# Kernel tuning notes

Measured on AMD Instinct MI355X. Metric: run time of the kernel, lower is better.

The kernel has to match this reference:

```python
import jax, jax.numpy as jnp
import numpy as np

N_NODES = 50000
N_EDGES = 1600000
NUM_GRAPHS = 512
HID = 128
EDGE_DIM = 64
N_CONV = 4
BN_EPS = 1e-5


def setup_inputs() -> dict:
    key = jax.random.key(0)
    ks = jax.random.split(key, 16)
    x = jax.random.normal(ks[0], (N_NODES, 9), dtype=jnp.float32)
    edge_index = jax.random.randint(ks[1], (2, N_EDGES), 0, N_NODES, dtype=jnp.int64)
    edge_attr = jax.random.normal(ks[2], (N_EDGES, EDGE_DIM), dtype=jnp.float32)
    batch = jnp.sort(jax.random.randint(ks[3], (N_NODES,), 0, NUM_GRAPHS, dtype=jnp.int64))
    s = 0.05
    W_emb = jax.random.normal(ks[4], (9, HID), dtype=jnp.float32) * s
    b_emb = jnp.zeros((HID,), jnp.float32)
    zin = 2 * HID + EDGE_DIM  # 320: cat([x_i, x_j, edge_attr])
    Wf = jax.random.normal(ks[5], (N_CONV, zin, HID), dtype=jnp.float32) * s
    bf = jnp.zeros((N_CONV, HID), jnp.float32)
    Ws = jax.random.normal(ks[6], (N_CONV, zin, HID), dtype=jnp.float32) * s
    bs = jnp.zeros((N_CONV, HID), jnp.float32)
    gamma = jnp.ones((N_CONV, HID), jnp.float32)
    beta = jnp.zeros((N_CONV, HID), jnp.float32)
    W1 = jax.random.normal(ks[7], (HID, HID // 2), dtype=jnp.float32) * s
    b1 = jnp.zeros((HID // 2,), jnp.float32)
    W2 = jax.random.normal(ks[8], (HID // 2, 1), dtype=jnp.float32) * s
    b2 = jnp.zeros((1,), jnp.float32)
    return dict(x=x, edge_index=edge_index, edge_attr=edge_attr, batch=batch,
                W_emb=W_emb, b_emb=b_emb, Wf=Wf, bf=bf, Ws=Ws, bs=bs,
                gamma=gamma, beta=beta, W1=W1, b1=b1, W2=W2, b2=b2)


def _segment_mean(vals, idx, num_segments):
    s = jax.ops.segment_sum(vals, idx, num_segments=num_segments)
    cnt = jax.ops.segment_sum(jnp.ones((vals.shape[0], 1), vals.dtype), idx,
                              num_segments=num_segments)
    return s / jnp.maximum(cnt, 1.0)


def _forward(x, edge_index, edge_attr, batch, W_emb, b_emb, Wf, bf, Ws, bs,
             gamma, beta, W1, b1, W2, b2):
    src, dst = edge_index[0], edge_index[1]  # x_j = x[src], x_i = x[dst]
    h = x @ W_emb + b_emb  # [N, HID]
    for l in range(N_CONV):
        residual = h
        # lin(cat([x_i, x_j, e])) == x_i@W[:H] + x_j@W[H:2H] + e@W[2H:] + b,
        # with node projections done at N granularity before the edge gather.
        f = (h @ Wf[l, :HID])[dst] + (h @ Wf[l, HID:2 * HID])[src] \
            + edge_attr @ Wf[l, 2 * HID:] + bf[l]
        g = (h @ Ws[l, :HID])[dst] + (h @ Ws[l, HID:2 * HID])[src] \
            + edge_attr @ Ws[l, 2 * HID:] + bs[l]
        msg = jax.nn.sigmoid(f) * jax.nn.softplus(g)  # [E, HID]
        aggr = _segment_mean(msg, dst, N_NODES)
        h_conv = aggr + h  # CGConv internal residual
        # BatchNorm1d (training-mode batch stats, biased variance)
        mu = jnp.mean(h_conv, axis=0)
        var = jnp.mean(jnp.square(h_conv - mu), axis=0)
        h_bn = gamma[l] * (h_conv - mu) * jax.lax.rsqrt(var + BN_EPS) + beta[l]
        h = jax.nn.relu(h_bn) + residual  # dropout = identity (eval)
    pooled = _segment_mean(h, batch, NUM_GRAPHS)  # [G, HID]
    out = jax.nn.softplus(pooled @ W1 + b1) @ W2 + b2
    return out.squeeze(-1)  # [G]


def reference(x, edge_index, edge_attr, batch, W_emb, b_emb, Wf, bf, Ws, bs,
              gamma, beta, W1, b1, W2, b2):
    return _forward(x, edge_index, edge_attr, batch, W_emb, b_emb, Wf, bf,
                    Ws, bs, gamma, beta, W1, b1, W2, b2)
```

## Files before the change

kernel.cpp:

```cpp
#include <hip/hip_runtime.h>
#include <math.h>

#define N_NODES 50000
#define N_EDGES 1600000
#define NGRAPH  512
#define HID     128
#define EDIM    64
#define NCONV   4

typedef __attribute__((ext_vector_type(8))) short short8;
typedef __attribute__((ext_vector_type(4))) float f32x4;
typedef unsigned int  u32;
typedef unsigned short u16;

#define MFMA16(a, b, c) __builtin_amdgcn_mfma_f32_16x16x32_bf16(a, b, c, 0, 0, 0)

__device__ __forceinline__ float fsig(float x) {
  return __builtin_amdgcn_rcpf(1.f + __expf(-x));
}
__device__ __forceinline__ float fsp(float x) {
  return fmaxf(x, 0.f) + __logf(1.f + __expf(-fabsf(x)));
}
__device__ __forceinline__ u16 f2bf(float x) {
  u32 u = __float_as_uint(x);
  return (u16)((u + 0x7fff + ((u >> 16) & 1)) >> 16);
}
__device__ __forceinline__ u32 f2bf_pack(float lo, float hi) {
  u32 a = __float_as_uint(lo), b = __float_as_uint(hi);
  u32 ra = (a + 0x7fff + ((a >> 16) & 1)) >> 16;
  u32 rb = (b + 0x7fff + ((b >> 16) & 1)) & 0xffff0000u;
  return ra | rb;
}
__device__ __forceinline__ short8 cvt8(float4 a, float4 b) {
  union { short8 s; u32 u[4]; } r;
  r.u[0] = f2bf_pack(a.x, a.y);
  r.u[1] = f2bf_pack(a.z, a.w);
  r.u[2] = f2bf_pack(b.x, b.y);
  r.u[3] = f2bf_pack(b.z, b.w);
  return r.s;
}

__global__ __launch_bounds__(256) void k_embed(const float* __restrict__ x,
                                               const float* __restrict__ Wemb,
                                               const float* __restrict__ bemb,
                                               float* __restrict__ h,
                                               u16* __restrict__ hb, u16* __restrict__ hlo) {
  int i = blockIdx.x * blockDim.x + threadIdx.x;
  if (i >= N_NODES * HID) return;
  int n = i >> 7, c = i & 127;
  const float* xr = x + (size_t)n * 9;
  float acc = bemb[c];
#pragma unroll
  for (int k = 0; k < 9; k++) acc = fmaf(xr[k], Wemb[k * HID + c], acc);
  h[i] = acc;
  u16 hi16 = f2bf(acc);
  hb[i] = hi16;
  hlo[i] = f2bf(acc - __uint_as_float((u32)hi16 << 16));
}

__global__ __launch_bounds__(256) void k_count(const int* __restrict__ ei, int* __restrict__ cnt) {
  int e = blockIdx.x * blockDim.x + threadIdx.x;
  if (e >= N_EDGES) return;
  atomicAdd(&cnt[ei[N_EDGES + e]], 1);
}

__global__ __launch_bounds__(256) void k_scan1(const int* __restrict__ cnt, int* __restrict__ bsum) {
  __shared__ int s[256];
  int i = blockIdx.x * 256 + threadIdx.x;
  s[threadIdx.x] = (i < N_NODES) ? cnt[i] : 0;
  __syncthreads();
  for (int o = 128; o > 0; o >>= 1) {
    if (threadIdx.x < o) s[threadIdx.x] += s[threadIdx.x + o];
    __syncthreads();
  }
  if (threadIdx.x == 0) bsum[blockIdx.x] = s[0];
}

__global__ __launch_bounds__(256) void k_scan2(int* __restrict__ bsum, int nb) {
  __shared__ int s[256];
  int tid = threadIdx.x;
  s[tid] = (tid < nb) ? bsum[tid] : 0;
  __syncthreads();
  for (int o = 1; o < 256; o <<= 1) {
    int t = (tid >= o) ? s[tid - o] : 0;
    __syncthreads();
    s[tid] += t;
    __syncthreads();
  }
  if (tid < nb) bsum[tid] = (tid == 0) ? 0 : s[tid - 1];
}

__global__ __launch_bounds__(256) void k_scan3(const int* __restrict__ cnt, const int* __restrict__ bsum,
                                               int* __restrict__ row_start, float* __restrict__ inv) {
  __shared__ int s[256];
  int i = blockIdx.x * 256 + threadIdx.x;
  int v = (i < N_NODES) ? cnt[i] : 0;
  s[threadIdx.x] = v;
  __syncthreads();
  for (int o = 1; o < 256; o <<= 1) {
    int t = (threadIdx.x >= o) ? s[threadIdx.x - o] : 0;
    __syncthreads();
    s[threadIdx.x] += t;
    __syncthreads();
  }
  if (i < N_NODES) {
    row_start[i + 1] = s[threadIdx.x] + bsum[blockIdx.x];
    inv[i] = 1.0f / (float)max(v, 1);
    if (i == 0) row_start[0] = 0;
  }
}

__global__ __launch_bounds__(256) void k_fill(const int* __restrict__ ei, const int* __restrict__ row_start,
                                              int* __restrict__ cur, int* __restrict__ eids,
                                              int* __restrict__ esrc) {
  int e = blockIdx.x * blockDim.x + threadIdx.x;
  if (e < 64) {
    eids[N_EDGES + e] = 0;
    esrc[N_EDGES + e] = 0;
  }
  if (e >= N_EDGES) return;
  int s = ei[e], d = ei[N_EDGES + e];
  int pos = row_start[d] + atomicAdd(&cur[d], 1);
  eids[pos] = e;
  esrc[pos] = s;
}

__global__ __launch_bounds__(256) void k_gatherA(const float* __restrict__ eattr,
                                                 const int* __restrict__ eids,
                                                 u16* __restrict__ Ae) {
  int t = blockIdx.x * 256 + threadIdx.x;
  if (t >= (N_EDGES + 64) * 8) return;
  int pos = t >> 3, chunk = t & 7;
  short8* dst = (short8*)((char*)Ae + ((size_t)pos << 7) + (chunk << 4));
  if (pos >= N_EDGES) {
    union { short8 s; u32 u[4]; } z; z.u[0] = z.u[1] = z.u[2] = z.u[3] = 0;
    *dst = z.s;
    return;
  }
  int eid = eids[pos];
  const float* src = eattr + ((size_t)eid << 6) + (chunk << 3);
  float4 a = *(const float4*)src;
  float4 b = *(const float4*)(src + 4);
  *dst = cvt8(a, b);
}

__global__ __launch_bounds__(256) void k_prepW(const float* __restrict__ Wf,
                                               const float* __restrict__ Ws,
                                               u16* __restrict__ Whi, u16* __restrict__ Wlo) {
  int t = blockIdx.x * 256 + threadIdx.x;
  if (t >= 65536 * NCONV) return;
  int l = t >> 16, t16 = t & 65535;
  int c = t16 >> 7, k = t16 & 127;
  int q = c >> 7, col = c & 127;
  const float* W = ((q < 2) ? Wf : Ws) + (size_t)l * 320 * HID;
  int row = (q & 1) ? (128 + k) : k;
  float wv = W[row * HID + col];
  u16 hb16 = f2bf(wv);
  float lo = wv - __uint_as_float((u32)hb16 << 16);
  int nt = (c >> 4) & 7, l15 = c & 15;
  int s = k >> 5, lg = (k >> 3) & 3, i = k & 7;
  int idx = l * 65536 + (((q * 8 + nt) * 4 + s) * 64 + (lg * 16 + l15)) * 8 + i;
  Whi[idx] = hb16;
  Wlo[idx] = f2bf(lo);
}

__global__ __launch_bounds__(256) void k_prepB(const float* __restrict__ Wf,
                                               const float* __restrict__ Ws,
                                               u16* __restrict__ Bhi) {
  int t = blockIdx.x * 256 + threadIdx.x;
  if (t >= 16384 * NCONV) return;
  int l = t >> 14, tid = t & 16383;
  int i = tid & 7, lane = (tid >> 3) & 63, s = (tid >> 9) & 1, nt = tid >> 10;
  int k = s * 32 + ((lane >> 4) << 3) + i;
  int col = ((nt & 7) << 4) + (lane & 15);
  const float* W = ((nt < 8) ? Wf : Ws) + (size_t)l * 320 * HID + 256 * HID;
  Bhi[t] = f2bf(W[k * HID + col]);
}

__global__ __launch_bounds__(256) void k_nodeproj_mfma(
    const u16* __restrict__ hb, const u16* __restrict__ hlo,
    const u16* __restrict__ Whi, const u16* __restrict__ Wlo,
    const float* __restrict__ bf_l, const float* __restrict__ bs_l,
    float* __restrict__ Pd, u32* __restrict__ Ppk) {
  const int lane = threadIdx.x & 63, w = threadIdx.x >> 6;
  const int l15 = lane & 15, lg = lane >> 4;
  const int nb = blockIdx.x * 16;
  const short8* WH = (const short8*)Whi;
  const short8* WL = (const short8*)Wlo;
  f32x4 acc[8];
#pragma unroll
  for (int nt = 0; nt < 8; nt++) acc[nt] = (f32x4){0.f, 0.f, 0.f, 0.f};
  const u32 arow = ((u32)(nb + l15)) << 8;
#pragma unroll
  for (int s = 0; s < 4; s++) {
    u32 ao = arow + (s << 6) + (lg << 4);
    short8 ah = *(const short8*)((const char*)hb + ao);
    short8 al = *(const short8*)((const char*)hlo + ao);
#pragma unroll
    for (int nt = 0; nt < 8; nt++) {
      int bi = ((w * 8 + nt) * 4 + s) * 64 + lane;
      short8 bhv = WH[bi];
      short8 blv = WL[bi];
      acc[nt] = MFMA16(ah, bhv, acc[nt]);
      acc[nt] = MFMA16(ah, blv, acc[nt]);
      acc[nt] = MFMA16(al, bhv, acc[nt]);
    }
  }
  if ((w & 1) == 0) {
    const float* bias = (w == 0) ? bf_l : bs_l;
    int pdoff = (w == 0) ? 0 : 128;
#pragma unroll
    for (int nt = 0; nt < 8; nt++) {
      int col = nt * 16 + l15;
      float b = bias[col];
#pragma unroll
      for (int r = 0; r < 4; r++) {
        int node = nb + lg * 4 + r;
        Pd[(size_t)node * 256 + pdoff + col] = acc[nt][r] + b;
      }
    }
  } else {
    int off = (w == 1) ? 0 : 1;
#pragma unroll
    for (int g = 0; g < 4; g++) {
#pragma unroll
      for (int r = 0; r < 4; r++) {
        int node = nb + lg * 4 + r;
        Ppk[(size_t)node * 128 + 2 * (g * 16 + l15) + off] =
            f2bf_pack(acc[2 * g][r], acc[2 * g + 1][r]);
      }
    }
  }
}

__global__ __launch_bounds__(256, 5) void k_edge_mfma(
    const float* __restrict__ Pd, const u32* __restrict__ Ppk,
    const float* __restrict__ h, const u16* __restrict__ Ae,
    const int* __restrict__ row_start, const float* __restrict__ inv,
    const int* __restrict__ esrc, const u16* __restrict__ Bhi,
    float* __restrict__ hconv, float* __restrict__ stats) {
  const int tid = threadIdx.x;
  const int lane = tid & 63;
  const int w = tid >> 6;
  const int l15 = lane & 15, lg = lane >> 4;
  const int cb = w * 32;

  const short8* BH = (const short8*)Bhi;
  short8 bh[4][2];
  const int nts[4] = {2 * w, 2 * w + 1, 8 + 2 * w, 9 + 2 * w};
#pragma unroll
  for (int t = 0; t < 4; t++) {
#pragma unroll
    for (int s = 0; s < 2; s++) bh[t][s] = BH[(nts[t] * 2 + s) * 64 + lane];
  }

  const u32 poff = ((u32)(w * 16 + l15)) << 3;
  const int eoff = lg << 2;
  const char* aeb = (const char*)Ae;
  const char* ppb = (const char*)Ppk;

  float st0s = 0.f, st0q = 0.f, st1s = 0.f, st1q = 0.f;

  for (int node = blockIdx.x; node < N_NODES; node += gridDim.x) {
    int rs = row_start[node], re = row_start[node + 1];
    int deg = re - rs;
    if (deg == 0) {
      if (lane < 32) {
        size_t idx = (size_t)node * HID + cb + lane;
        float v = h[idx];
        hconv[idx] = v;
        if (lane < 16) { st0s += v; st0q += v * v; }
        else           { st1s += v; st1q += v * v; }
      }
      continue;
    }
    const float* Pn = Pd + (size_t)node * 256;
    float fd0 = Pn[cb + l15];
    float fd1 = Pn[cb + 16 + l15];
    float gd0 = Pn[128 + cb + l15];
    float gd1 = Pn[128 + cb + 16 + l15];
    float acc0 = 0.f, acc1 = 0.f;
    int ntile = (deg + 15) >> 4;

    const int* ep = esrc + rs + eoff;
    int sn0 = ep[0], sn1 = ep[1], sn2 = ep[2], sn3 = ep[3];
    uint2 gc0 = *(const uint2*)(ppb + (((u32)sn0) << 9) + poff);
    uint2 gc1 = *(const uint2*)(ppb + (((u32)sn1) << 9) + poff);
    uint2 gc2 = *(const uint2*)(ppb + (((u32)sn2) << 9) + poff);
    uint2 gc3 = *(const uint2*)(ppb + (((u32)sn3) << 9) + poff);
    sn0 = ep[16]; sn1 = ep[17]; sn2 = ep[18]; sn3 = ep[19];
    u32 ab = ((u32)(rs + l15) << 7) + ((u32)lg << 4);
    short8 ac0 = *(const short8*)(aeb + ab);
    short8 ac1 = *(const short8*)(aeb + ab + 64);

    for (int mt = 0; mt < ntile; mt++) {
      uint2 gn0 = *(const uint2*)(ppb + (((u32)sn0) << 9) + poff);
      uint2 gn1 = *(const uint2*)(ppb + (((u32)sn1) << 9) + poff);
      uint2 gn2 = *(const uint2*)(ppb + (((u32)sn2) << 9) + poff);
      uint2 gn3 = *(const uint2*)(ppb + (((u32)sn3) << 9) + poff);
      int t2 = (mt + 2) * 16;
      sn0 = ep[t2 + 0]; sn1 = ep[t2 + 1]; sn2 = ep[t2 + 2]; sn3 = ep[t2 + 3];

      f32x4 d0 = {fd0, fd0, fd0, fd0};
      f32x4 d1 = {fd1, fd1, fd1, fd1};
      f32x4 d2 = {gd0, gd0, gd0, gd0};
      f32x4 d3 = {gd1, gd1, gd1, gd1};
      d0 = MFMA16(ac0, bh[0][0], d0); d0 = MFMA16(ac1, bh[0][1], d0);
      d1 = MFMA16(ac0, bh[1][0], d1); d1 = MFMA16(ac1, bh[1][1], d1);
      d2 = MFMA16(ac0, bh[2][0], d2); d2 = MFMA16(ac1, bh[2][1], d2);
      d3 = MFMA16(ac0, bh[3][0], d3); d3 = MFMA16(ac1, bh[3][1], d3);

      u32 ab1 = ab + (u32)(mt + 1) * 2048;
      ac0 = *(const short8*)(aeb + ab1);
      ac1 = *(const short8*)(aeb + ab1 + 64);

      const uint2 pgr[4] = {gc0, gc1, gc2, gc3};
      bool fullt = ((mt + 1) * 16 <= deg);
#pragma unroll
      for (int r = 0; r < 4; r++) {
        uint2 pg = pgr[r];
        float f0 = d0[r] + __uint_as_float(pg.x << 16);
        float f1 = d1[r] + __uint_as_float(pg.x & 0xffff0000u);
        float g0 = d2[r] + __uint_as_float(pg.y << 16);
        float g1 = d3[r] + __uint_as_float(pg.y & 0xffff0000u);
        float m0 = fsig(f0) * fsp(g0);
        float m1 = fsig(f1) * fsp(g1);
        if (!fullt) {
          int row = mt * 16 + (lg << 2) + r;
          if (row >= deg) { m0 = 0.f; m1 = 0.f; }
        }
        acc0 += m0;
        acc1 += m1;
      }
      gc0 = gn0; gc1 = gn1; gc2 = gn2; gc3 = gn3;
    }
    acc0 += __shfl_xor(acc0, 16); acc0 += __shfl_xor(acc0, 32);
    acc1 += __shfl_xor(acc1, 16); acc1 += __shfl_xor(acc1, 32);
    float iv = inv[node];
    if (lane < 16) {
      size_t idx = (size_t)node * HID + cb + lane;
      float v = acc0 * iv + h[idx];
      hconv[idx] = v;
      st0s += v; st0q += v * v;
    } else if (lane < 32) {
      size_t idx = (size_t)node * HID + cb + 16 + l15;
      float v = acc1 * iv + h[idx];
      hconv[idx] = v;
      st1s += v; st1q += v * v;
    }
  }
  if (lane < 16) {
    atomicAdd(&stats[cb + lane], st0s);
    atomicAdd(&stats[128 + cb + lane], st0q);
  } else if (lane < 32) {
    atomicAdd(&stats[cb + 16 + l15], st1s);
    atomicAdd(&stats[128 + cb + 16 + l15], st1q);
  }
}

__global__ __launch_bounds__(256) void k_bn3(const float* __restrict__ hconv, float* __restrict__ h,
                                             const float* __restrict__ stats,
                                             const float* __restrict__ gamma,
                                             const float* __restrict__ beta,
                                             u16* __restrict__ hb, u16* __restrict__ hlo) {
  __shared__ float ssl[256];
  int t = threadIdx.x;
  if (t < 128) {
    float mu = stats[t] * (1.f / N_NODES);
    float var = stats[128 + t] * (1.f / N_NODES) - mu * mu;
    float sc = gamma[t] * rsqrtf(var + 1e-5f);
    ssl[t] = sc;
    ssl[128 + t] = beta[t] - mu * sc;
  }
  __syncthreads();
  int i = blockIdx.x * 256 + t;
  if (i >= N_NODES * HID) return;
  int c = i & 127;
  float v = hconv[i] * ssl[c] + ssl[128 + c];
  float hn = fmaxf(v, 0.f) + h[i];
  h[i] = hn;
  u16 hi16 = f2bf(hn);
  hb[i] = hi16;
  hlo[i] = f2bf(hn - __uint_as_float((u32)hi16 << 16));
}

__global__ __launch_bounds__(128) void k_pool(const float* __restrict__ h, const int* __restrict__ batch,
                                              float* __restrict__ pooled) {
  int g = blockIdx.x;
  int c = threadIdx.x;
  int lo = 0, hi = N_NODES;
  while (lo < hi) { int m = (lo + hi) >> 1; if (batch[m] < g) lo = m + 1; else hi = m; }
  int s = lo;
  lo = 0; hi = N_NODES;
  while (lo < hi) { int m = (lo + hi) >> 1; if (batch[m] < g + 1) lo = m + 1; else hi = m; }
  int e = lo;
  float acc = 0.f;
  for (int n = s; n < e; n++) acc += h[(size_t)n * HID + c];
  pooled[(size_t)g * HID + c] = acc / (float)max(e - s, 1);
}

__global__ __launch_bounds__(64) void k_head(const float* __restrict__ pooled, const float* __restrict__ W1,
                                             const float* __restrict__ b1, const float* __restrict__ W2,
                                             const float* __restrict__ b2, float* __restrict__ out) {
  int g = blockIdx.x;
  int j = threadIdx.x;
  float acc = b1[j];
#pragma unroll 16
  for (int k = 0; k < 128; k++) acc = fmaf(pooled[(size_t)g * HID + k], W1[k * 64 + j], acc);
  float z = fmaxf(acc, 0.f) + __logf(1.f + __expf(-fabsf(acc)));
  float v = z * W2[j];
  for (int o = 32; o > 0; o >>= 1) v += __shfl_down(v, o);
  if (j == 0) out[g] = v + b2[0];
}

extern "C" void kernel_launch(void* const* d_in, const int* in_sizes, int n_in,
                              void* d_out, int out_size, void* d_ws, size_t ws_size,
                              hipStream_t stream) {
  const float* x     = (const float*)d_in[0];
  const int*   ei    = (const int*)d_in[1];
  const float* eattr = (const float*)d_in[2];
  const int*   batch = (const int*)d_in[3];
  const float* Wemb  = (const float*)d_in[4];
  const float* bemb  = (const float*)d_in[5];
  const float* Wf    = (const float*)d_in[6];
  const float* bf    = (const float*)d_in[7];
  const float* Ws    = (const float*)d_in[8];
  const float* bs    = (const float*)d_in[9];
  const float* gamma = (const float*)d_in[10];
  const float* beta  = (const float*)d_in[11];
  const float* W1    = (const float*)d_in[12];
  const float* b1    = (const float*)d_in[13];
  const float* W2    = (const float*)d_in[14];
  const float* b2    = (const float*)d_in[15];
  float* out = (float*)d_out;

  char* ws = (char*)d_ws;
  size_t off = 0;
  auto alloc = [&](size_t bytes) -> char* {
    char* p = ws + off;
    off += (bytes + 255) & ~(size_t)255;
    return p;
  };
  float* h         = (float*)alloc((size_t)N_NODES * HID * 4);
  u16*   hb        = (u16*)alloc((size_t)N_NODES * HID * 2);
  u16*   hlo       = (u16*)alloc((size_t)N_NODES * HID * 2);
  float* Pd        = (float*)alloc((size_t)N_NODES * 256 * 4);
  u32*   Ppk       = (u32*)alloc((size_t)N_NODES * 128 * 4);
  float* hconv     = (float*)alloc((size_t)N_NODES * HID * 4);
  int*   row_start = (int*)alloc((size_t)(N_NODES + 1) * 4);
  float* inv       = (float*)alloc((size_t)N_NODES * 4);
  int*   eids      = (int*)alloc((size_t)(N_EDGES + 64) * 4);
  int*   esrc      = (int*)alloc((size_t)(N_EDGES + 64) * 4);
  u16*   Ae        = (u16*)alloc((size_t)(N_EDGES + 64) * EDIM * 2);
  u16*   Bhi       = (u16*)alloc((size_t)16384 * NCONV * 2);
  u16*   Whi       = (u16*)alloc((size_t)65536 * NCONV * 2);
  u16*   Wlo       = (u16*)alloc((size_t)65536 * NCONV * 2);
  char*  zbase     = ws + off;
  int*   cnt       = (int*)alloc((size_t)N_NODES * 4);
  int*   cur       = (int*)alloc((size_t)N_NODES * 4);
  float* stats     = (float*)alloc((size_t)NCONV * 256 * 4);
  size_t zbytes    = (size_t)((ws + off) - zbase);
  int*   bsum      = (int*)alloc(256 * 4);
  float* pooled    = (float*)alloc((size_t)NGRAPH * HID * 4);
  (void)ws_size; (void)in_sizes; (void)n_in; (void)out_size;

  hipMemsetAsync(zbase, 0, zbytes, stream);

  k_embed<<<(N_NODES * HID + 255) / 256, 256, 0, stream>>>(x, Wemb, bemb, h, hb, hlo);

  k_count<<<(N_EDGES + 255) / 256, 256, 0, stream>>>(ei, cnt);
  int nb = (N_NODES + 255) / 256;
  k_scan1<<<nb, 256, 0, stream>>>(cnt, bsum);
  k_scan2<<<1, 256, 0, stream>>>(bsum, nb);
  k_scan3<<<nb, 256, 0, stream>>>(cnt, bsum, row_start, inv);
  k_fill<<<(N_EDGES + 255) / 256, 256, 0, stream>>>(ei, row_start, cur, eids, esrc);
  k_gatherA<<<((N_EDGES + 64) * 8 + 255) / 256, 256, 0, stream>>>(eattr, eids, Ae);
  k_prepW<<<65536 * NCONV / 256, 256, 0, stream>>>(Wf, Ws, Whi, Wlo);
  k_prepB<<<16384 * NCONV / 256, 256, 0, stream>>>(Wf, Ws, Bhi);

  for (int l = 0; l < NCONV; l++) {
    k_nodeproj_mfma<<<N_NODES / 16, 256, 0, stream>>>(hb, hlo, Whi + l * 65536, Wlo + l * 65536,
                                                      bf + l * HID, bs + l * HID, Pd, Ppk);
    k_edge_mfma<<<2560, 256, 0, stream>>>(Pd, Ppk, h, Ae, row_start, inv, esrc,
                                          Bhi + l * 16384, hconv, stats + l * 256);
    k_bn3<<<(N_NODES * HID + 255) / 256, 256, 0, stream>>>(hconv, h, stats + l * 256,
                                                           gamma + l * HID, beta + l * HID,
                                                           hb, hlo);
  }

  k_pool<<<NGRAPH, HID, 0, stream>>>(h, batch, pooled);
  k_head<<<NGRAPH, 64, 0, stream>>>(pooled, W1, b1, W2, b2, out);
}
```

Before: 2.192 ms.

## Balance edge kernel with 16-edge tile worklist and atomic aggregation

Replaces the per-node grid-stride edge loop with a precomputed worklist of 16-edge tiles, built once per forward by scan kernels. Each block then gets a contiguous, equal-sized chunk of tiles, which removes load imbalance from varying node degree. Partial sums are flushed with atomics into a zeroed aggr buffer, and a separate k_stats kernel applies the mean, adds the residual and computes BN statistics. The cost is an extra memset and an extra pass over hconv per layer, atomic traffic at node boundaries, and a lower occupancy hint.

```diff
diff --git a/kernel.cpp b/kernel.cpp
--- a/kernel.cpp
+++ b/kernel.cpp
@@ -7,6 +7,7 @@
 #define HID     128
 #define EDIM    64
 #define NCONV   4
+#define MAXWI   150064
 
 typedef __attribute__((ext_vector_type(8))) short short8;
 typedef __attribute__((ext_vector_type(4))) float f32x4;
@@ -123,6 +124,55 @@
   int pos = row_start[d] + atomicAdd(&cur[d], 1);
   eids[pos] = e;
   esrc[pos] = s;
+}
+
+__global__ __launch_bounds__(256) void k_tilecnt(const int* __restrict__ row_start,
+                                                 int* __restrict__ tcnt) {
+  int i = blockIdx.x * 256 + threadIdx.x;
+  if (i >= N_NODES) return;
+  tcnt[i] = (row_start[i + 1] - row_start[i] + 15) >> 4;
+}
+
+__global__ __launch_bounds__(256) void k_scan3w(const int* __restrict__ tcnt,
+                                                const int* __restrict__ bsum,
+                                                int* __restrict__ tstart) {
+  __shared__ int s[256];
+  int i = blockIdx.x * 256 + threadIdx.x;
+  int v = (i < N_NODES) ? tcnt[i] : 0;
+  s[threadIdx.x] = v;
+  __syncthreads();
+  for (int o = 1; o < 256; o <<= 1) {
+    int t = (threadIdx.x >= o) ? s[threadIdx.x - o] : 0;
+    __syncthreads();
+    s[threadIdx.x] += t;
+    __syncthreads();
+  }
+  if (i < N_NODES) {
+    tstart[i] = s[threadIdx.x] - v + bsum[blockIdx.x];
+    if (i == N_NODES - 1) tstart[N_NODES] = s[threadIdx.x] + bsum[blockIdx.x];
+  }
+}
+
+__global__ __launch_bounds__(256) void k_wfill(const int* __restrict__ row_start,
+                                               const int* __restrict__ tstart,
+                                               int* __restrict__ wnode, int* __restrict__ wbase) {
+  int n = blockIdx.x * 256 + threadIdx.x;
+  if (n >= N_NODES) return;
+  int rs = row_start[n], re = row_start[n + 1];
+  int ts = tstart[n];
+  int nt = (re - rs + 15) >> 4;
+  for (int mt = 0; mt < nt; ++mt) {
+    wnode[ts + mt] = n;
+    wbase[ts + mt] = rs + mt * 16;
+  }
+}
+
+__global__ void k_wpad(const int* __restrict__ tstart,
+                       int* __restrict__ wnode, int* __restrict__ wbase) {
+  int t = threadIdx.x;
+  int nwi = tstart[N_NODES];
+  wnode[nwi + t] = 0;
+  wbase[nwi + t] = 0;
 }
 
 __global__ __launch_bounds__(256) void k_gatherA(const float* __restrict__ eattr,
@@ -233,18 +283,24 @@
   }
 }
 
-__global__ __launch_bounds__(256, 5) void k_edge_mfma(
+__global__ __launch_bounds__(256, 4) void k_edge_wl(
     const float* __restrict__ Pd, const u32* __restrict__ Ppk,
-    const float* __restrict__ h, const u16* __restrict__ Ae,
-    const int* __restrict__ row_start, const float* __restrict__ inv,
+    const u16* __restrict__ Ae, const int* __restrict__ row_start,
     const int* __restrict__ esrc, const u16* __restrict__ Bhi,
-    float* __restrict__ hconv, float* __restrict__ stats) {
+    const int* __restrict__ wnode, const int* __restrict__ wbase,
+    const int* __restrict__ tstart, float* __restrict__ aggr) {
   const int tid = threadIdx.x;
   const int lane = tid & 63;
   const int w = tid >> 6;
   const int l15 = lane & 15, lg = lane >> 4;
   const int cb = w * 32;
 
+  const int NWI = tstart[N_NODES];
+  int C = (NWI + (int)gridDim.x - 1) / (int)gridDim.x;
+  int k0 = (int)blockIdx.x * C;
+  int k1 = min(k0 + C, NWI);
+  if (k0 >= k1) return;
+
   const short8* BH = (const short8*)Bhi;
   short8 bh[4][2];
   const int nts[4] = {2 * w, 2 * w + 1, 8 + 2 * w, 9 + 2 * w};
@@ -259,102 +315,114 @@
   const char* aeb = (const char*)Ae;
   const char* ppb = (const char*)Ppk;
 
-  float st0s = 0.f, st0q = 0.f, st1s = 0.f, st1q = 0.f;
-
-  for (int node = blockIdx.x; node < N_NODES; node += gridDim.x) {
-    int rs = row_start[node], re = row_start[node + 1];
-    int deg = re - rs;
-    if (deg == 0) {
-      if (lane < 32) {
-        size_t idx = (size_t)node * HID + cb + lane;
-        float v = h[idx];
-        hconv[idx] = v;
-        if (lane < 16) { st0s += v; st0q += v * v; }
-        else           { st1s += v; st1q += v * v; }
+  int wn0 = wnode[k0],     wb0 = wbase[k0];
+  int wn1 = wnode[k0 + 1], wb1 = wbase[k0 + 1];
+  int wn2 = wnode[k0 + 2], wb2 = wbase[k0 + 2];
+  int re0 = row_start[wn0 + 1];
+  const float* Pn0 = Pd + (size_t)wn0 * 256;
+  float fd0 = Pn0[cb + l15], fd1 = Pn0[cb + 16 + l15];
+  float gd0 = Pn0[128 + cb + l15], gd1 = Pn0[128 + cb + 16 + l15];
+  uint2 gc0, gc1, gc2, gc3;
+  {
+    const int* ep0 = esrc + wb0 + eoff;
+    int a = ep0[0], b = ep0[1], c2 = ep0[2], d = ep0[3];
+    gc0 = *(const uint2*)(ppb + (((u32)a) << 9) + poff);
+    gc1 = *(const uint2*)(ppb + (((u32)b) << 9) + poff);
+    gc2 = *(const uint2*)(ppb + (((u32)c2) << 9) + poff);
+    gc3 = *(const uint2*)(ppb + (((u32)d) << 9) + poff);
+  }
+  const int* ep1 = esrc + wb1 + eoff;
+  int sA0 = ep1[0], sA1 = ep1[1], sA2 = ep1[2], sA3 = ep1[3];
+  u32 ab = ((u32)(wb0 + l15) << 7) + ((u32)lg << 4);
+  short8 ac0 = *(const short8*)(aeb + ab);
+  short8 ac1 = *(const short8*)(aeb + ab + 64);
+
+  float acc0 = 0.f, acc1 = 0.f;
+
+  for (int k = k0; k < k1; ++k) {
+    uint2 gn0 = *(const uint2*)(ppb + (((u32)sA0) << 9) + poff);
+    uint2 gn1 = *(const uint2*)(ppb + (((u32)sA1) << 9) + poff);
+    uint2 gn2 = *(const uint2*)(ppb + (((u32)sA2) << 9) + poff);
+    uint2 gn3 = *(const uint2*)(ppb + (((u32)sA3) << 9) + poff);
+    int wn3 = wnode[k + 3], wb3 = wbase[k + 3];
+    const int* ep2 = esrc + wb2 + eoff;
+    int t0 = ep2[0], t1 = ep2[1], t2 = ep2[2], t3 = ep2[3];
+    int re1 = row_start[wn1 + 1];
+    const float* Pn1 = Pd + (size_t)wn1 * 256;
+    float nfd0 = Pn1[cb + l15], nfd1 = Pn1[cb + 16 + l15];
+    float ngd0 = Pn1[128 + cb + l15], ngd1 = Pn1[128 + cb + 16 + l15];
+
+    f32x4 d0 = {fd0, fd0, fd0, fd0};
+    f32x4 d1 = {fd1, fd1, fd1, fd1};
+    f32x4 d2 = {gd0, gd0, gd0, gd0};
+    f32x4 d3 = {gd1, gd1, gd1, gd1};
+    d0 = MFMA16(ac0, bh[0][0], d0); d0 = MFMA16(ac1, bh[0][1], d0);
+    d1 = MFMA16(ac0, bh[1][0], d1); d1 = MFMA16(ac1, bh[1][1], d1);
+    d2 = MFMA16(ac0, bh[2][0], d2); d2 = MFMA16(ac1, bh[2][1], d2);
+    d3 = MFMA16(ac0, bh[3][0], d3); d3 = MFMA16(ac1, bh[3][1], d3);
+
+    u32 ab1 = ((u32)(wb1 + l15) << 7) + ((u32)lg << 4);
+    ac0 = *(const short8*)(aeb + ab1);
+    ac1 = *(const short8*)(aeb + ab1 + 64);
+
+    const uint2 pgr[4] = {gc0, gc1, gc2, gc3};
+    int rowlim = re0 - wb0;
+    bool fullt = (rowlim >= 16);
+#pragma unroll
+    for (int r = 0; r < 4; r++) {
+      uint2 pg = pgr[r];
+      float f0 = d0[r] + __uint_as_float(pg.x << 16);
+      float f1 = d1[r] + __uint_as_float(pg.x & 0xffff0000u);
+      float g0 = d2[r] + __uint_as_float(pg.y << 16);
+      float g1 = d3[r] + __uint_as_float(pg.y & 0xffff0000u);
+      float m0 = fsig(f0) * fsp(g0);
+      float m1 = fsig(f1) * fsp(g1);
+      if (!fullt) {
+        int row = (lg << 2) + r;
+        if (row >= rowlim) { m0 = 0.f; m1 = 0.f; }
       }
-      continue;
+      acc0 += m0;
+      acc1 += m1;
     }
-    const float* Pn = Pd + (size_t)node * 256;
-    float fd0 = Pn[cb + l15];
-    float fd1 = Pn[cb + 16 + l15];
-    float gd0 = Pn[128 + cb + l15];
-    float gd1 = Pn[128 + cb + 16 + l15];
-    float acc0 = 0.f, acc1 = 0.f;
-    int ntile = (deg + 15) >> 4;
-
-    const int* ep = esrc + rs + eoff;
-    int sn0 = ep[0], sn1 = ep[1], sn2 = ep[2], sn3 = ep[3];
-    uint2 gc0 = *(const uint2*)(ppb + (((u32)sn0) << 9) + poff);
-    uint2 gc1 = *(const uint2*)(ppb + (((u32)sn1) << 9) + poff);
-    uint2 gc2 = *(const uint2*)(ppb + (((u32)sn2) << 9) + poff);
-    uint2 gc3 = *(const uint2*)(ppb + (((u32)sn3) << 9) + poff);
-    sn0 = ep[16]; sn1 = ep[17]; sn2 = ep[18]; sn3 = ep[19];
-    u32 ab = ((u32)(rs + l15) << 7) + ((u32)lg << 4);
-    short8 ac0 = *(const short8*)(aeb + ab);
-    short8 ac1 = *(const short8*)(aeb + ab + 64);
-
-    for (int mt = 0; mt < ntile; mt++) {
-      uint2 gn0 = *(const uint2*)(ppb + (((u32)sn0) << 9) + poff);
-      uint2 gn1 = *(const uint2*)(ppb + (((u32)sn1) << 9) + poff);
-      uint2 gn2 = *(const uint2*)(ppb + (((u32)sn2) << 9) + poff);
-      uint2 gn3 = *(const uint2*)(ppb + (((u32)sn3) << 9) + poff);
-      int t2 = (mt + 2) * 16;
-      sn0 = ep[t2 + 0]; sn1 = ep[t2 + 1]; sn2 = ep[t2 + 2]; sn3 = ep[t2 + 3];
-
-      f32x4 d0 = {fd0, fd0, fd0, fd0};
-      f32x4 d1 = {fd1, fd1, fd1, fd1};
-      f32x4 d2 = {gd0, gd0, gd0, gd0};
-      f32x4 d3 = {gd1, gd1, gd1, gd1};
-      d0 = MFMA16(ac0, bh[0][0], d0); d0 = MFMA16(ac1, bh[0][1], d0);
-      d1 = MFMA16(ac0, bh[1][0], d1); d1 = MFMA16(ac1, bh[1][1], d1);
-      d2 = MFMA16(ac0, bh[2][0], d2); d2 = MFMA16(ac1, bh[2][1], d2);
-      d3 = MFMA16(ac0, bh[3][0], d3); d3 = MFMA16(ac1, bh[3][1], d3);
-
-      u32 ab1 = ab + (u32)(mt + 1) * 2048;
-      ac0 = *(const short8*)(aeb + ab1);
-      ac1 = *(const short8*)(aeb + ab1 + 64);
-
-      const uint2 pgr[4] = {gc0, gc1, gc2, gc3};
-      bool fullt = ((mt + 1) * 16 <= deg);
-#pragma unroll
-      for (int r = 0; r < 4; r++) {
-        uint2 pg = pgr[r];
-        float f0 = d0[r] + __uint_as_float(pg.x << 16);
-        float f1 = d1[r] + __uint_as_float(pg.x & 0xffff0000u);
-        float g0 = d2[r] + __uint_as_float(pg.y << 16);
-        float g1 = d3[r] + __uint_as_float(pg.y & 0xffff0000u);
-        float m0 = fsig(f0) * fsp(g0);
-        float m1 = fsig(f1) * fsp(g1);
-        if (!fullt) {
-          int row = mt * 16 + (lg << 2) + r;
-          if (row >= deg) { m0 = 0.f; m1 = 0.f; }
-        }
-        acc0 += m0;
-        acc1 += m1;
+
+    if (wn0 != wn1 || k == k1 - 1) {
+      acc0 += __shfl_xor(acc0, 16); acc0 += __shfl_xor(acc0, 32);
+      acc1 += __shfl_xor(acc1, 16); acc1 += __shfl_xor(acc1, 32);
+      if (lane < 16) {
+        atomicAdd(&aggr[(size_t)wn0 * HID + cb + lane], acc0);
+      } else if (lane < 32) {
+        atomicAdd(&aggr[(size_t)wn0 * HID + cb + 16 + l15], acc1);
       }
-      gc0 = gn0; gc1 = gn1; gc2 = gn2; gc3 = gn3;
+      acc0 = 0.f; acc1 = 0.f;
     }
-    acc0 += __shfl_xor(acc0, 16); acc0 += __shfl_xor(acc0, 32);
-    acc1 += __shfl_xor(acc1, 16); acc1 += __shfl_xor(acc1, 32);
-    float iv = inv[node];
-    if (lane < 16) {
-      size_t idx = (size_t)node * HID + cb + lane;
-      float v = acc0 * iv + h[idx];
-      hconv[idx] = v;
-      st0s += v; st0q += v * v;
-    } else if (lane < 32) {
-      size_t idx = (size_t)node * HID + cb + 16 + l15;
-      float v = acc1 * iv + h[idx];
-      hconv[idx] = v;
-      st1s += v; st1q += v * v;
-    }
-  }
-  if (lane < 16) {
-    atomicAdd(&stats[cb + lane], st0s);
-    atomicAdd(&stats[128 + cb + lane], st0q);
-  } else if (lane < 32) {
-    atomicAdd(&stats[cb + 16 + l15], st1s);
-    atomicAdd(&stats[128 + cb + 16 + l15], st1q);
+
+    wn0 = wn1; wb0 = wb1; wn1 = wn2; wb1 = wb2; wn2 = wn3; wb2 = wb3;
+    re0 = re1;
+    fd0 = nfd0; fd1 = nfd1; gd0 = ngd0; gd1 = ngd1;
+    gc0 = gn0; gc1 = gn1; gc2 = gn2; gc3 = gn3;
+    sA0 = t0; sA1 = t1; sA2 = t2; sA3 = t3;
+  }
+}
+
+__global__ __launch_bounds__(256) void k_stats(float* __restrict__ hconv,
+                                               const float* __restrict__ h,
+                                               const float* __restrict__ inv,
+                                               float* __restrict__ stats) {
+  __shared__ float sb[512];
+  int c = threadIdx.x & 127;
+  float s1 = 0.f, s2 = 0.f;
+  for (int i = blockIdx.x * 256 + threadIdx.x; i < N_NODES * HID; i += gridDim.x * 256) {
+    float v = hconv[i] * inv[i >> 7] + h[i];
+    hconv[i] = v;
+    s1 += v;
+    s2 += v * v;
+  }
+  sb[threadIdx.x] = s1;
+  sb[256 + threadIdx.x] = s2;
+  __syncthreads();
+  if (threadIdx.x < 128) {
+    atomicAdd(&stats[c], sb[threadIdx.x] + sb[threadIdx.x + 128]);
+    atomicAdd(&stats[128 + c], sb[256 + threadIdx.x] + sb[256 + threadIdx.x + 128]);
   }
 }
 
@@ -455,6 +523,11 @@
   u16*   Bhi       = (u16*)alloc((size_t)16384 * NCONV * 2);
   u16*   Whi       = (u16*)alloc((size_t)65536 * NCONV * 2);
   u16*   Wlo       = (u16*)alloc((size_t)65536 * NCONV * 2);
+  int*   tcnt      = (int*)alloc((size_t)N_NODES * 4);
+  int*   tstart    = (int*)alloc((size_t)(N_NODES + 1) * 4);
+  int*   wnode     = (int*)alloc((size_t)MAXWI * 4);
+  int*   wbase     = (int*)alloc((size_t)MAXWI * 4);
+  int*   bsum2     = (int*)alloc(256 * 4);
   char*  zbase     = ws + off;
   int*   cnt       = (int*)alloc((size_t)N_NODES * 4);
   int*   cur       = (int*)alloc((size_t)N_NODES * 4);
@@ -475,14 +548,24 @@
   k_scan3<<<nb, 256, 0, stream>>>(cnt, bsum, row_start, inv);
   k_fill<<<(N_EDGES + 255) / 256, 256, 0, stream>>>(ei, row_start, cur, eids, esrc);
   k_gatherA<<<((N_EDGES + 64) * 8 + 255) / 256, 256, 0, stream>>>(eattr, eids, Ae);
+
+  k_tilecnt<<<nb, 256, 0, stream>>>(row_start, tcnt);
+  k_scan1<<<nb, 256, 0, stream>>>(tcnt, bsum2);
+  k_scan2<<<1, 256, 0, stream>>>(bsum2, nb);
+  k_scan3w<<<nb, 256, 0, stream>>>(tcnt, bsum2, tstart);
+  k_wfill<<<nb, 256, 0, stream>>>(row_start, tstart, wnode, wbase);
+  k_wpad<<<1, 64, 0, stream>>>(tstart, wnode, wbase);
+
   k_prepW<<<65536 * NCONV / 256, 256, 0, stream>>>(Wf, Ws, Whi, Wlo);
   k_prepB<<<16384 * NCONV / 256, 256, 0, stream>>>(Wf, Ws, Bhi);
 
   for (int l = 0; l < NCONV; l++) {
     k_nodeproj_mfma<<<N_NODES / 16, 256, 0, stream>>>(hb, hlo, Whi + l * 65536, Wlo + l * 65536,
                                                       bf + l * HID, bs + l * HID, Pd, Ppk);
-    k_edge_mfma<<<2560, 256, 0, stream>>>(Pd, Ppk, h, Ae, row_start, inv, esrc,
-                                          Bhi + l * 16384, hconv, stats + l * 256);
+    hipMemsetAsync(hconv, 0, (size_t)N_NODES * HID * 4, stream);
+    k_edge_wl<<<2560, 256, 0, stream>>>(Pd, Ppk, Ae, row_start, esrc,
+                                        Bhi + l * 16384, wnode, wbase, tstart, hconv);
+    k_stats<<<128, 256, 0, stream>>>(hconv, h, inv, stats + l * 256);
     k_bn3<<<(N_NODES * HID + 255) / 256, 256, 0, stream>>>(hconv, h, stats + l * 256,
                                                            gamma + l * HID, beta + l * HID,
                                                            hb, hlo);
```

After: 2.061 ms. -6.0%, faster.
